# Kernel tuning notes

Hardware: AMD Instinct MI355X
Metric: run time of the kernel (lower is better)

The kernel has to match this reference:

```python
import jax, jax.numpy as jnp
import numpy as np

# Constants from the module source
F_LEN = 1000.0          # focal length (init kwarg f)
C_PP = 512.0            # principal point (init kwarg c)
CAM_SIZE = 1024.0       # camera image_size
H_IMG, W_IMG = 1920 // 8, 1080 // 8   # raster image_size = (240, 135)
SIGMA = 1e-4            # BlendParams.sigma
BLUR = float(np.log(1.0 / 1e-4 - 1.0) * 1e-4)  # blur_radius
V, F = 600, 1000


def setup_inputs() -> dict:
    key = jax.random.key(0)
    k1, k2, k3 = jax.random.split(key, 3)
    # place mesh in front of camera (z ~ 2.5) so it projects on-screen
    verts = jax.random.normal(k1, (V, 3), dtype=jnp.float32) * 0.3 + jnp.array([0.0, 0.0, 2.5], jnp.float32)
    faces = jax.random.randint(k2, (F, 3), 0, V, dtype=jnp.int32)
    gt = (jax.random.uniform(k3, (H_IMG, W_IMG)) > 0.5).astype(jnp.float32)
    return {"verts": verts, "gt": gt, "faces": faces}


def _soft_silhouette(verts, faces):
    # verts: [V,3] camera-space after R flip; faces: [F,3] int
    R = jnp.array([[-1.0, 0.0, 0.0], [0.0, -1.0, 0.0], [0.0, 0.0, 1.0]], verts.dtype)
    v = verts @ R.T                              # == (R @ verts.T).T
    z = jnp.maximum(v[:, 2], 1e-6)
    # pinhole projection to 1024x1024 camera pixels, rescaled to raster grid
    px = (F_LEN * v[:, 0] / z + C_PP) / CAM_SIZE * W_IMG
    py = (F_LEN * v[:, 1] / z + C_PP) / CAM_SIZE * H_IMG
    v2 = jnp.stack([px, py], axis=-1)            # [V,2] raster-pixel coords
    tri = v2[faces]                              # [F,3,2]
    tz = v[:, 2][faces].mean(axis=-1)            # [F] mean depth per face

    ys = jnp.arange(H_IMG, dtype=verts.dtype) + 0.5
    xs = jnp.arange(W_IMG, dtype=verts.dtype) + 0.5
    gy, gx = jnp.meshgrid(ys, xs, indexing="ij")
    p = jnp.stack([gx.ravel(), gy.ravel()], axis=-1)[:, None, :]  # [P,1,2]

    d2min = jnp.full((H_IMG * W_IMG, F), jnp.inf, verts.dtype)
    pos = jnp.ones((H_IMG * W_IMG, F), bool)
    neg = jnp.ones((H_IMG * W_IMG, F), bool)
    for k in range(3):  # fixed loop over 3 triangle edges
        a = tri[None, :, k, :]                   # [1,F,2]
        b = tri[None, :, (k + 1) % 3, :]
        ab = b - a                               # [1,F,2]
        ap = p - a                               # [P,F,2]
        cross = ab[..., 0] * ap[..., 1] - ab[..., 1] * ap[..., 0]
        pos = pos & (cross >= 0)
        neg = neg & (cross <= 0)
        t = jnp.clip((ap * ab).sum(-1) / ((ab * ab).sum(-1) + 1e-12), 0.0, 1.0)
        d2 = ((ap - t[..., None] * ab) ** 2).sum(-1)  # sq dist to edge segment
        d2min = jnp.minimum(d2min, d2)

    inside = pos | neg                           # point-in-triangle test
    signed_d2 = jnp.where(inside, -d2min, d2min) # pytorch3d signed sq distance
    prob = jax.nn.sigmoid(-signed_d2 / SIGMA)    # per-face coverage prob
    valid = (tz > 1e-6)[None, :] & (inside | (d2min <= BLUR))
    prob = jnp.where(valid, prob, 0.0)
    # SoftSilhouetteShader: alpha = 1 - prod_f (1 - prob_f), stable in log space
    alpha = 1.0 - jnp.exp(jnp.sum(jnp.log1p(-prob), axis=1))
    return alpha.reshape(H_IMG, W_IMG)


def reference(verts, gt, faces):
    sil = _soft_silhouette(verts, faces)
    loss = jnp.mean(jnp.abs(sil - gt))
    return loss, sil
```

## Files before the change

### kernel.cpp

```cpp
#include <hip/hip_runtime.h>
#include <math.h>

#define HI 240
#define WI 135
#define NPIX (HI * WI)
#define NF 1000
#define NCHUNK 10
#define FCHUNK (NF / NCHUNK)
#define BLK 256
#define FREC 4
#define TW 8
#define TH 8
#define TX_N 17
#define TY_N 30
#define NTILE (TX_N * TY_N)
#define TPB 4
#define NBX ((NTILE + TPB - 1) / TPB)


__device__ __forceinline__ void project(float x, float y, float z,
                                        float& px, float& py) {
#pragma clang fp contract(off)
    float zc = fmaxf(z, 1e-6f);
    px = ((1000.0f * (-x)) / zc + 512.0f) / 1024.0f * (float)WI;
    py = ((1000.0f * (-y)) / zc + 512.0f) / 1024.0f * (float)HI;
}

__device__ __forceinline__ float eval_face(const float4* sf, int f,
                                           float px, float py)
{
    float4 r0v = sf[FREC * f + 0];
    float4 r1v = sf[FREC * f + 1];
    float4 r2v = sf[FREC * f + 2];
    float4 dv  = sf[FREC * f + 3];

    float a0x = px - r0v.x, a0y = py - r0v.y;
    float a1x = px - r1v.x, a1y = py - r1v.y;
    float a2x = px - r2v.x, a2y = py - r2v.y;

    float c0, c1, c2;
    {
#pragma clang fp contract(off)
        c0 = r0v.z * a0y - r0v.w * a0x;
        c1 = r1v.z * a1y - r1v.w * a1x;
        c2 = r2v.z * a2y - r2v.w * a2x;
    }
    bool pos = (c0 >= 0.0f) & (c1 >= 0.0f) & (c2 >= 0.0f);
    bool neg = (c0 <= 0.0f) & (c1 <= 0.0f) & (c2 <= 0.0f);

    float t0 = fminf(fmaxf((a0x * r0v.z + a0y * r0v.w) * dv.x, 0.0f), 1.0f);
    float t1 = fminf(fmaxf((a1x * r1v.z + a1y * r1v.w) * dv.y, 0.0f), 1.0f);
    float t2 = fminf(fmaxf((a2x * r2v.z + a2y * r2v.w) * dv.z, 0.0f), 1.0f);
    float u0x = a0x - t0 * r0v.z, u0y = a0y - t0 * r0v.w;
    float u1x = a1x - t1 * r1v.z, u1y = a1y - t1 * r1v.w;
    float u2x = a2x - t2 * r2v.z, u2y = a2y - t2 * r2v.w;
    float d20 = u0x * u0x + u0y * u0y;
    float d21 = u1x * u1x + u1y * u1y;
    float d22 = u2x * u2x + u2y * u2y;
    float d2m = fminf(d20, fminf(d21, d22));

    bool inside = pos | neg;
    float uu = (inside ? d2m : -d2m) * 1.0e4f;
    bool valid = (dv.w != 0.0f) & (inside | (d2m <= 9.2102404e-4f));
    float sp;
    if (uu > 16.0f) sp = uu;
    else sp = fmaxf(uu, 0.0f) + __logf(1.0f + __expf(-fabsf(uu)));
    return valid ? sp : 0.0f;
}

__global__ __launch_bounds__(BLK) void sil_kernel(
    const float* __restrict__ verts, const int* __restrict__ faces,
    float* __restrict__ ws, float* __restrict__ out)
{
    __shared__ float4 sf[FCHUNK * FREC];
    __shared__ float sbx0[FCHUNK], sby0[FCHUNK], sbx1[FCHUNK], sby1[FCHUNK];
    __shared__ float sPx[3][FCHUNK], sPy[3][FCHUNK];
    __shared__ float sEx[3][FCHUNK], sEy[3][FCHUNK];
    __shared__ float sRd[3][FCHUNK];
    __shared__ float sFlag[FCHUNK];

    if (blockIdx.x == 0 && blockIdx.y == 0 && threadIdx.x == 0) out[0] = 0.0f;

    {
        int f = threadIdx.x;
        if (f < FCHUNK) {
#pragma clang fp contract(off)
            int g = blockIdx.y * FCHUNK + f;
            int i0 = faces[3 * g + 0], i1 = faces[3 * g + 1], i2 = faces[3 * g + 2];
            float x0 = verts[3 * i0 + 0], y0 = verts[3 * i0 + 1], z0 = verts[3 * i0 + 2];
            float x1 = verts[3 * i1 + 0], y1 = verts[3 * i1 + 1], z1 = verts[3 * i1 + 2];
            float x2 = verts[3 * i2 + 0], y2 = verts[3 * i2 + 1], z2 = verts[3 * i2 + 2];

            float p0x, p0y, p1x, p1y, p2x, p2y;
            project(x0, y0, z0, p0x, p0y);
            project(x1, y1, z1, p1x, p1y);
            project(x2, y2, z2, p2x, p2y);

            float e0x = p1x - p0x, e0y = p1y - p0y;
            float e1x = p2x - p1x, e1y = p2y - p1y;
            float e2x = p0x - p2x, e2y = p0y - p2y;
            float den0 = (e0x * e0x + e0y * e0y) + 1e-12f;
            float den1 = (e1x * e1x + e1y * e1y) + 1e-12f;
            float den2 = (e2x * e2x + e2y * e2y) + 1e-12f;
            float rd0 = 1.0f / den0, rd1 = 1.0f / den1, rd2 = 1.0f / den2;

            float tz = ((z0 + z1) + z2) / 3.0f;
            bool tzok = tz > 1e-6f;

            float orient = e0x * e1y - e0y * e1x;
            float area2 = fabsf(orient);
            float l2max = fmaxf(den0, fmaxf(den1, den2));
            bool dup = (i0 == i1) || (i1 == i2) || (i2 == i0);
            bool patho = dup || (area2 < 4.0e-3f * l2max) || (l2max > 4.0e6f);

            float bx0, by0, bx1, by1, flag;
            if (!tzok) {
                bx0 = 1e30f; by0 = 1e30f; bx1 = -1e30f; by1 = -1e30f; flag = 0.0f;
            } else if (patho) {
                bx0 = -1e30f; by0 = -1e30f; bx1 = 1e30f; by1 = 1e30f; flag = 2.0f;
            } else {
                bx0 = fminf(p0x, fminf(p1x, p2x)) - 0.3f;
                by0 = fminf(p0y, fminf(p1y, p2y)) - 0.3f;
                bx1 = fmaxf(p0x, fmaxf(p1x, p2x)) + 0.3f;
                by1 = fmaxf(p0y, fmaxf(p1y, p2y)) + 0.3f;
                flag = 1.0f;
            }

            sf[FREC * f + 0] = make_float4(p0x, p0y, e0x, e0y);
            sf[FREC * f + 1] = make_float4(p1x, p1y, e1x, e1y);
            sf[FREC * f + 2] = make_float4(p2x, p2y, e2x, e2y);
            sf[FREC * f + 3] = make_float4(rd0, rd1, rd2, tzok ? 1.0f : 0.0f);
            sbx0[f] = bx0; sby0[f] = by0; sbx1[f] = bx1; sby1[f] = by1;
            sFlag[f] = flag;
            float sgn = (orient >= 0.0f) ? 1.0f : -1.0f;
            sPx[0][f] = p0x; sPy[0][f] = p0y; sEx[0][f] = sgn * e0x; sEy[0][f] = sgn * e0y; sRd[0][f] = rd0;
            sPx[1][f] = p1x; sPy[1][f] = p1y; sEx[1][f] = sgn * e1x; sEy[1][f] = sgn * e1y; sRd[1][f] = rd1;
            sPx[2][f] = p2x; sPy[2][f] = p2y; sEx[2][f] = sgn * e2x; sEy[2][f] = sgn * e2y; sRd[2][f] = rd2;
        }
    }
    __syncthreads();

    int wave = threadIdx.x >> 6, lane = threadIdx.x & 63;
    int tile = blockIdx.x * TPB + wave;
    if (tile >= NTILE) return;

    int ty = tile / TX_N, tx = tile - ty * TX_N;
    int col = tx * TW + (lane & 7);
    int row = ty * TH + (lane >> 3);
    bool live = col < WI;
    int q = row * WI + col;
    float px = (float)col + 0.5f;
    float py = (float)row + 0.5f;
    float wx0 = (float)(tx * TW) + 0.5f, wx1 = (float)(tx * TW + TW - 1) + 0.5f;
    float wy0 = (float)(ty * TH) + 0.5f, wy1 = (float)(ty * TH + TH - 1) + 0.5f;

    float sum = live ? 0.0f : -1e30f;
    bool done = false;

    for (int r = 0; r < (FCHUNK + 63) / 64 && !done; ++r) {
        int fl = r * 64 + lane;
        bool ov = false;
        if (fl < FCHUNK) {
            ov = !(sbx0[fl] > wx1 || sbx1[fl] < wx0 ||
                   sby0[fl] > wy1 || sby1[fl] < wy0);
            if (ov && sFlag[fl] == 1.0f) {
                bool cull = false;
#pragma unroll
                for (int k = 0; k < 3; ++k) {
                    float Ex = sEx[k][fl], Ey = sEy[k][fl];
                    float base = Ex * (wy0 - sPy[k][fl]) - Ey * (wx0 - sPx[k][fl]);
                    float mx = base + fmaxf(0.0f, -7.0f * Ey)
                                    + fmaxf(0.0f,  7.0f * Ex);
                    cull |= (mx < 0.0f) & (mx * mx * sRd[k][fl] > 0.09f);
                }
                ov = !cull;
            }
        }
        unsigned long long m = __ballot(ov);

        while (m) {
            int f0 = __ffsll((long long)m) - 1;
            m &= m - 1;
            bool has1 = (m != 0);
            int f1 = has1 ? (__ffsll((long long)m) - 1) : f0;
            if (has1) m &= m - 1;

            float s0 = eval_face(sf, r * 64 + f0, px, py);
            float s1 = eval_face(sf, r * 64 + f1, px, py);
            sum -= s0 + (has1 ? s1 : 0.0f);

            if (__ballot(sum <= -30.0f) == 0xFFFFFFFFFFFFFFFFull) {
                done = true;
                break;
            }
        }
    }
    if (live) ws[(size_t)blockIdx.y * NPIX + q] = sum;
}

__global__ __launch_bounds__(BLK) void fin_kernel(
    const float* __restrict__ ws, const float* __restrict__ gt,
    float* __restrict__ out)
{
    __shared__ float wsum[BLK / 64];
    int q = blockIdx.x * BLK + threadIdx.x;
    float c = 0.0f;
    if (q < NPIX) {
        float s = 0.0f;
        for (int ch = 0; ch < NCHUNK; ++ch) s += ws[(size_t)ch * NPIX + q];
        float alpha = 1.0f - __expf(s);
        out[1 + q] = alpha;
        c = fabsf(alpha - gt[q]);
    }
    for (int off = 32; off > 0; off >>= 1) c += __shfl_down(c, off, 64);
    if ((threadIdx.x & 63) == 0) wsum[threadIdx.x >> 6] = c;
    __syncthreads();
    if (threadIdx.x == 0) {
        float s = 0.0f;
        for (int w = 0; w < BLK / 64; ++w) s += wsum[w];
        atomicAdd(&out[0], s * (1.0f / (float)NPIX));
    }
}

extern "C" void kernel_launch(void* const* d_in, const int* in_sizes, int n_in,
                              void* d_out, int out_size, void* d_ws, size_t ws_size,
                              hipStream_t stream)
{
    const float* verts = (const float*)d_in[0];
    const float* gt    = (const float*)d_in[1];
    const int*   faces = (const int*)d_in[2];
    float* out = (float*)d_out;
    float* ws  = (float*)d_ws;

    dim3 sgrid(NBX, NCHUNK);
    sil_kernel<<<sgrid, BLK, 0, stream>>>(verts, faces, ws, out);

    fin_kernel<<<(NPIX + BLK - 1) / BLK, BLK, 0, stream>>>(ws, gt, out);
}
```

Baseline: 72.41 us.

## Hoist face setup into a prep kernel and double face chunks per pixel tile

Face projection and bounding-box setup move out of every sil_kernel block into a separate prep kernel, which writes per-chunk records to global memory. Each block now just copies its chunk into shared memory. NCHUNK doubles to 20, so each block handles 50 faces in a single 64-lane ballot pass and the grid has twice as many blocks. This removes redundant per-block setup work and adds parallelism, at the cost of one extra kernel launch and twice the workspace traffic in fin_kernel.

New measurement: 77.96 us. 7.7% more time.

```diff
diff --git a/kernel.cpp b/kernel.cpp
--- a/kernel.cpp
+++ b/kernel.cpp
@@ -5,7 +5,7 @@
 #define WI 135
 #define NPIX (HI * WI)
 #define NF 1000
-#define NCHUNK 10
+#define NCHUNK 20
 #define FCHUNK (NF / NCHUNK)
 #define BLK 256
 #define FREC 4
@@ -17,6 +17,11 @@
 #define TPB 4
 #define NBX ((NTILE + TPB - 1) / TPB)
 
+#define CH_EVAL (FCHUNK * FREC)
+#define NSCAN 20
+#define CH_SCAN_F (NSCAN * FCHUNK)
+#define CH_SCAN_V (CH_SCAN_F / 4)
+
 
 __device__ __forceinline__ void project(float x, float y, float z,
                                         float& px, float& py) {
@@ -24,6 +29,74 @@
     float zc = fmaxf(z, 1e-6f);
     px = ((1000.0f * (-x)) / zc + 512.0f) / 1024.0f * (float)WI;
     py = ((1000.0f * (-y)) / zc + 512.0f) / 1024.0f * (float)HI;
+}
+
+__global__ __launch_bounds__(BLK) void prep_kernel(
+    const float* __restrict__ verts, const int* __restrict__ faces,
+    float* __restrict__ out, float4* __restrict__ gA, float* __restrict__ gS)
+{
+#pragma clang fp contract(off)
+    int g = blockIdx.x * BLK + threadIdx.x;
+    if (g == 0) out[0] = 0.0f;
+    if (g >= NF) return;
+
+    int i0 = faces[3 * g + 0], i1 = faces[3 * g + 1], i2 = faces[3 * g + 2];
+    float x0 = verts[3 * i0 + 0], y0 = verts[3 * i0 + 1], z0 = verts[3 * i0 + 2];
+    float x1 = verts[3 * i1 + 0], y1 = verts[3 * i1 + 1], z1 = verts[3 * i1 + 2];
+    float x2 = verts[3 * i2 + 0], y2 = verts[3 * i2 + 1], z2 = verts[3 * i2 + 2];
+
+    float p0x, p0y, p1x, p1y, p2x, p2y;
+    project(x0, y0, z0, p0x, p0y);
+    project(x1, y1, z1, p1x, p1y);
+    project(x2, y2, z2, p2x, p2y);
+
+    float e0x = p1x - p0x, e0y = p1y - p0y;
+    float e1x = p2x - p1x, e1y = p2y - p1y;
+    float e2x = p0x - p2x, e2y = p0y - p2y;
+    float den0 = (e0x * e0x + e0y * e0y) + 1e-12f;
+    float den1 = (e1x * e1x + e1y * e1y) + 1e-12f;
+    float den2 = (e2x * e2x + e2y * e2y) + 1e-12f;
+    float rd0 = 1.0f / den0, rd1 = 1.0f / den1, rd2 = 1.0f / den2;
+
+    float tz = ((z0 + z1) + z2) / 3.0f;
+    bool tzok = tz > 1e-6f;
+
+    float orient = e0x * e1y - e0y * e1x;
+    float area2 = fabsf(orient);
+    float l2max = fmaxf(den0, fmaxf(den1, den2));
+    bool dup = (i0 == i1) || (i1 == i2) || (i2 == i0);
+    bool patho = dup || (area2 < 4.0e-3f * l2max) || (l2max > 4.0e6f);
+
+    float bx0, by0, bx1, by1, flag;
+    if (!tzok) {
+        bx0 = 1e30f; by0 = 1e30f; bx1 = -1e30f; by1 = -1e30f; flag = 0.0f;
+    } else if (patho) {
+        bx0 = -1e30f; by0 = -1e30f; bx1 = 1e30f; by1 = 1e30f; flag = 2.0f;
+    } else {
+        bx0 = fminf(p0x, fminf(p1x, p2x)) - 0.3f;
+        by0 = fminf(p0y, fminf(p1y, p2y)) - 0.3f;
+        bx1 = fmaxf(p0x, fmaxf(p1x, p2x)) + 0.3f;
+        by1 = fmaxf(p0y, fmaxf(p1y, p2y)) + 0.3f;
+        flag = 1.0f;
+    }
+
+    int c = g / FCHUNK, f = g - c * FCHUNK;
+    float4* ga = gA + (size_t)c * CH_EVAL;
+    ga[4 * f + 0] = make_float4(p0x, p0y, e0x, e0y);
+    ga[4 * f + 1] = make_float4(p1x, p1y, e1x, e1y);
+    ga[4 * f + 2] = make_float4(p2x, p2y, e2x, e2y);
+    ga[4 * f + 3] = make_float4(rd0, rd1, rd2, tzok ? 1.0f : 0.0f);
+
+    float* gs = gS + (size_t)c * CH_SCAN_F;
+    float sgn = (orient >= 0.0f) ? 1.0f : -1.0f;
+    gs[0 * FCHUNK + f] = bx0;  gs[1 * FCHUNK + f] = by0;
+    gs[2 * FCHUNK + f] = bx1;  gs[3 * FCHUNK + f] = by1;
+    gs[4 * FCHUNK + f] = flag;
+    gs[5 * FCHUNK + f] = p0x;  gs[6 * FCHUNK + f] = p1x;  gs[7 * FCHUNK + f] = p2x;
+    gs[8 * FCHUNK + f] = p0y;  gs[9 * FCHUNK + f] = p1y;  gs[10 * FCHUNK + f] = p2y;
+    gs[11 * FCHUNK + f] = sgn * e0x; gs[12 * FCHUNK + f] = sgn * e1x; gs[13 * FCHUNK + f] = sgn * e2x;
+    gs[14 * FCHUNK + f] = sgn * e0y; gs[15 * FCHUNK + f] = sgn * e1y; gs[16 * FCHUNK + f] = sgn * e2y;
+    gs[17 * FCHUNK + f] = rd0; gs[18 * FCHUNK + f] = rd1; gs[19 * FCHUNK + f] = rd2;
 }
 
 __device__ __forceinline__ float eval_face(const float4* sf, int f,
@@ -69,73 +142,19 @@
 }
 
 __global__ __launch_bounds__(BLK) void sil_kernel(
-    const float* __restrict__ verts, const int* __restrict__ faces,
-    float* __restrict__ ws, float* __restrict__ out)
-{
-    __shared__ float4 sf[FCHUNK * FREC];
-    __shared__ float sbx0[FCHUNK], sby0[FCHUNK], sbx1[FCHUNK], sby1[FCHUNK];
-    __shared__ float sPx[3][FCHUNK], sPy[3][FCHUNK];
-    __shared__ float sEx[3][FCHUNK], sEy[3][FCHUNK];
-    __shared__ float sRd[3][FCHUNK];
-    __shared__ float sFlag[FCHUNK];
-
-    if (blockIdx.x == 0 && blockIdx.y == 0 && threadIdx.x == 0) out[0] = 0.0f;
+    const float4* __restrict__ gA, const float* __restrict__ gS,
+    float* __restrict__ ws)
+{
+    __shared__ float4 sf[CH_EVAL];
+    __shared__ float4 sscan4[CH_SCAN_V];
+    const float* ss = (const float*)sscan4;
 
     {
-        int f = threadIdx.x;
-        if (f < FCHUNK) {
-#pragma clang fp contract(off)
-            int g = blockIdx.y * FCHUNK + f;
-            int i0 = faces[3 * g + 0], i1 = faces[3 * g + 1], i2 = faces[3 * g + 2];
-            float x0 = verts[3 * i0 + 0], y0 = verts[3 * i0 + 1], z0 = verts[3 * i0 + 2];
-            float x1 = verts[3 * i1 + 0], y1 = verts[3 * i1 + 1], z1 = verts[3 * i1 + 2];
-            float x2 = verts[3 * i2 + 0], y2 = verts[3 * i2 + 1], z2 = verts[3 * i2 + 2];
-
-            float p0x, p0y, p1x, p1y, p2x, p2y;
-            project(x0, y0, z0, p0x, p0y);
-            project(x1, y1, z1, p1x, p1y);
-            project(x2, y2, z2, p2x, p2y);
-
-            float e0x = p1x - p0x, e0y = p1y - p0y;
-            float e1x = p2x - p1x, e1y = p2y - p1y;
-            float e2x = p0x - p2x, e2y = p0y - p2y;
-            float den0 = (e0x * e0x + e0y * e0y) + 1e-12f;
-            float den1 = (e1x * e1x + e1y * e1y) + 1e-12f;
-            float den2 = (e2x * e2x + e2y * e2y) + 1e-12f;
-            float rd0 = 1.0f / den0, rd1 = 1.0f / den1, rd2 = 1.0f / den2;
-
-            float tz = ((z0 + z1) + z2) / 3.0f;
-            bool tzok = tz > 1e-6f;
-
-            float orient = e0x * e1y - e0y * e1x;
-            float area2 = fabsf(orient);
-            float l2max = fmaxf(den0, fmaxf(den1, den2));
-            bool dup = (i0 == i1) || (i1 == i2) || (i2 == i0);
-            bool patho = dup || (area2 < 4.0e-3f * l2max) || (l2max > 4.0e6f);
-
-            float bx0, by0, bx1, by1, flag;
-            if (!tzok) {
-                bx0 = 1e30f; by0 = 1e30f; bx1 = -1e30f; by1 = -1e30f; flag = 0.0f;
-            } else if (patho) {
-                bx0 = -1e30f; by0 = -1e30f; bx1 = 1e30f; by1 = 1e30f; flag = 2.0f;
-            } else {
-                bx0 = fminf(p0x, fminf(p1x, p2x)) - 0.3f;
-                by0 = fminf(p0y, fminf(p1y, p2y)) - 0.3f;
-                bx1 = fmaxf(p0x, fmaxf(p1x, p2x)) + 0.3f;
-                by1 = fmaxf(p0y, fmaxf(p1y, p2y)) + 0.3f;
-                flag = 1.0f;
-            }
-
-            sf[FREC * f + 0] = make_float4(p0x, p0y, e0x, e0y);
-            sf[FREC * f + 1] = make_float4(p1x, p1y, e1x, e1y);
-            sf[FREC * f + 2] = make_float4(p2x, p2y, e2x, e2y);
-            sf[FREC * f + 3] = make_float4(rd0, rd1, rd2, tzok ? 1.0f : 0.0f);
-            sbx0[f] = bx0; sby0[f] = by0; sbx1[f] = bx1; sby1[f] = by1;
-            sFlag[f] = flag;
-            float sgn = (orient >= 0.0f) ? 1.0f : -1.0f;
-            sPx[0][f] = p0x; sPy[0][f] = p0y; sEx[0][f] = sgn * e0x; sEy[0][f] = sgn * e0y; sRd[0][f] = rd0;
-            sPx[1][f] = p1x; sPy[1][f] = p1y; sEx[1][f] = sgn * e1x; sEy[1][f] = sgn * e1y; sRd[1][f] = rd1;
-            sPx[2][f] = p2x; sPy[2][f] = p2y; sEx[2][f] = sgn * e2x; sEy[2][f] = sgn * e2y; sRd[2][f] = rd2;
+        const float4* ga = gA + (size_t)blockIdx.y * CH_EVAL;
+        const float4* gs4 = (const float4*)gS + (size_t)blockIdx.y * CH_SCAN_V;
+        for (int i = threadIdx.x; i < CH_EVAL + CH_SCAN_V; i += BLK) {
+            if (i < CH_EVAL) sf[i] = ga[i];
+            else             sscan4[i - CH_EVAL] = gs4[i - CH_EVAL];
         }
     }
     __syncthreads();
@@ -155,45 +174,41 @@
     float wy0 = (float)(ty * TH) + 0.5f, wy1 = (float)(ty * TH + TH - 1) + 0.5f;
 
     float sum = live ? 0.0f : -1e30f;
-    bool done = false;
-
-    for (int r = 0; r < (FCHUNK + 63) / 64 && !done; ++r) {
-        int fl = r * 64 + lane;
-        bool ov = false;
-        if (fl < FCHUNK) {
-            ov = !(sbx0[fl] > wx1 || sbx1[fl] < wx0 ||
-                   sby0[fl] > wy1 || sby1[fl] < wy0);
-            if (ov && sFlag[fl] == 1.0f) {
-                bool cull = false;
+
+    bool ov = false;
+    if (lane < FCHUNK) {
+        int fl = lane;
+        ov = !(ss[0 * FCHUNK + fl] > wx1 || ss[2 * FCHUNK + fl] < wx0 ||
+               ss[1 * FCHUNK + fl] > wy1 || ss[3 * FCHUNK + fl] < wy0);
+        if (ov && ss[4 * FCHUNK + fl] == 1.0f) {
+            bool cull = false;
 #pragma unroll
-                for (int k = 0; k < 3; ++k) {
-                    float Ex = sEx[k][fl], Ey = sEy[k][fl];
-                    float base = Ex * (wy0 - sPy[k][fl]) - Ey * (wx0 - sPx[k][fl]);
-                    float mx = base + fmaxf(0.0f, -7.0f * Ey)
-                                    + fmaxf(0.0f,  7.0f * Ex);
-                    cull |= (mx < 0.0f) & (mx * mx * sRd[k][fl] > 0.09f);
-                }
-                ov = !cull;
+            for (int k = 0; k < 3; ++k) {
+                float Ex = ss[(11 + k) * FCHUNK + fl];
+                float Ey = ss[(14 + k) * FCHUNK + fl];
+                float base = Ex * (wy0 - ss[(8 + k) * FCHUNK + fl])
+                           - Ey * (wx0 - ss[(5 + k) * FCHUNK + fl]);
+                float mx = base + fmaxf(0.0f, -7.0f * Ey)
+                                + fmaxf(0.0f,  7.0f * Ex);
+                cull |= (mx < 0.0f) & (mx * mx * ss[(17 + k) * FCHUNK + fl] > 0.09f);
             }
+            ov = !cull;
         }
-        unsigned long long m = __ballot(ov);
-
-        while (m) {
-            int f0 = __ffsll((long long)m) - 1;
-            m &= m - 1;
-            bool has1 = (m != 0);
-            int f1 = has1 ? (__ffsll((long long)m) - 1) : f0;
-            if (has1) m &= m - 1;
-
-            float s0 = eval_face(sf, r * 64 + f0, px, py);
-            float s1 = eval_face(sf, r * 64 + f1, px, py);
-            sum -= s0 + (has1 ? s1 : 0.0f);
-
-            if (__ballot(sum <= -30.0f) == 0xFFFFFFFFFFFFFFFFull) {
-                done = true;
-                break;
-            }
-        }
+    }
+    unsigned long long m = __ballot(ov);
+
+    while (m) {
+        int f0 = __ffsll((long long)m) - 1;
+        m &= m - 1;
+        bool has1 = (m != 0);
+        int f1 = has1 ? (__ffsll((long long)m) - 1) : f0;
+        if (has1) m &= m - 1;
+
+        float s0 = eval_face(sf, f0, px, py);
+        float s1 = eval_face(sf, f1, px, py);
+        sum -= s0 + (has1 ? s1 : 0.0f);
+
+        if (__ballot(sum <= -30.0f) == 0xFFFFFFFFFFFFFFFFull) break;
     }
     if (live) ws[(size_t)blockIdx.y * NPIX + q] = sum;
 }
@@ -230,10 +245,16 @@
     const float* gt    = (const float*)d_in[1];
     const int*   faces = (const int*)d_in[2];
     float* out = (float*)d_out;
-    float* ws  = (float*)d_ws;
+
+    char* w = (char*)d_ws;
+    float* ws = (float*)w;
+    float4* gA = (float4*)(w + (size_t)NCHUNK * NPIX * 4);
+    float* gS  = (float*)((char*)gA + (size_t)NF * FREC * 16);
+
+    prep_kernel<<<(NF + BLK - 1) / BLK, BLK, 0, stream>>>(verts, faces, out, gA, gS);
 
     dim3 sgrid(NBX, NCHUNK);
-    sil_kernel<<<sgrid, BLK, 0, stream>>>(verts, faces, ws, out);
+    sil_kernel<<<sgrid, BLK, 0, stream>>>(gA, gS, ws);
 
     fin_kernel<<<(NPIX + BLK - 1) / BLK, BLK, 0, stream>>>(ws, gt, out);
 }
```

## Process all faces per block and fuse alpha/loss into silhouette kernel

Applied to the files above, without the earlier changes.

Drops the split of faces into 10 chunks across grid y. Each block now projects and bins all 1000 faces into a 14-row SoA shared array and runs the whole face loop per tile. It then computes alpha and the per-pixel abs error directly, writes per-block partial sums, and a one-block kernel does a deterministic final reduction without atomics. Edges are recomputed from vertices in eval_face to save shared memory. This removes the workspace round-trip and gives early termination across all faces, but cuts grid parallelism tenfold (128 blocks instead of 1280) and makes every block redo projection for all faces.

Measured after the change: 86.83 us. 19.9% more time.

```diff
diff --git a/kernel.cpp b/kernel.cpp
--- a/kernel.cpp
+++ b/kernel.cpp
@@ -5,10 +5,7 @@
 #define WI 135
 #define NPIX (HI * WI)
 #define NF 1000
-#define NCHUNK 10
-#define FCHUNK (NF / NCHUNK)
 #define BLK 256
-#define FREC 4
 #define TW 8
 #define TH 8
 #define TX_N 17
@@ -26,34 +23,38 @@
     py = ((1000.0f * (-y)) / zc + 512.0f) / 1024.0f * (float)HI;
 }
 
-__device__ __forceinline__ float eval_face(const float4* sf, int f,
+__device__ __forceinline__ float eval_face(const float S[14][NF], int f,
                                            float px, float py)
 {
-    float4 r0v = sf[FREC * f + 0];
-    float4 r1v = sf[FREC * f + 1];
-    float4 r2v = sf[FREC * f + 2];
-    float4 dv  = sf[FREC * f + 3];
-
-    float a0x = px - r0v.x, a0y = py - r0v.y;
-    float a1x = px - r1v.x, a1y = py - r1v.y;
-    float a2x = px - r2v.x, a2y = py - r2v.y;
+    float p0x = S[5][f], p0y = S[6][f];
+    float p1x = S[7][f], p1y = S[8][f];
+    float p2x = S[9][f], p2y = S[10][f];
+    float rd0 = S[11][f], rd1 = S[12][f], rd2 = S[13][f];
+
+    float e0x = p1x - p0x, e0y = p1y - p0y;
+    float e1x = p2x - p1x, e1y = p2y - p1y;
+    float e2x = p0x - p2x, e2y = p0y - p2y;
+
+    float a0x = px - p0x, a0y = py - p0y;
+    float a1x = px - p1x, a1y = py - p1y;
+    float a2x = px - p2x, a2y = py - p2y;
 
     float c0, c1, c2;
     {
 #pragma clang fp contract(off)
-        c0 = r0v.z * a0y - r0v.w * a0x;
-        c1 = r1v.z * a1y - r1v.w * a1x;
-        c2 = r2v.z * a2y - r2v.w * a2x;
+        c0 = e0x * a0y - e0y * a0x;
+        c1 = e1x * a1y - e1y * a1x;
+        c2 = e2x * a2y - e2y * a2x;
     }
     bool pos = (c0 >= 0.0f) & (c1 >= 0.0f) & (c2 >= 0.0f);
     bool neg = (c0 <= 0.0f) & (c1 <= 0.0f) & (c2 <= 0.0f);
 
-    float t0 = fminf(fmaxf((a0x * r0v.z + a0y * r0v.w) * dv.x, 0.0f), 1.0f);
-    float t1 = fminf(fmaxf((a1x * r1v.z + a1y * r1v.w) * dv.y, 0.0f), 1.0f);
-    float t2 = fminf(fmaxf((a2x * r2v.z + a2y * r2v.w) * dv.z, 0.0f), 1.0f);
-    float u0x = a0x - t0 * r0v.z, u0y = a0y - t0 * r0v.w;
-    float u1x = a1x - t1 * r1v.z, u1y = a1y - t1 * r1v.w;
-    float u2x = a2x - t2 * r2v.z, u2y = a2y - t2 * r2v.w;
+    float t0 = fminf(fmaxf((a0x * e0x + a0y * e0y) * rd0, 0.0f), 1.0f);
+    float t1 = fminf(fmaxf((a1x * e1x + a1y * e1y) * rd1, 0.0f), 1.0f);
+    float t2 = fminf(fmaxf((a2x * e2x + a2y * e2y) * rd2, 0.0f), 1.0f);
+    float u0x = a0x - t0 * e0x, u0y = a0y - t0 * e0y;
+    float u1x = a1x - t1 * e1x, u1y = a1y - t1 * e1y;
+    float u2x = a2x - t2 * e2x, u2y = a2y - t2 * e2y;
     float d20 = u0x * u0x + u0y * u0y;
     float d21 = u1x * u1x + u1y * u1y;
     float d22 = u2x * u2x + u2y * u2y;
@@ -61,7 +62,7 @@
 
     bool inside = pos | neg;
     float uu = (inside ? d2m : -d2m) * 1.0e4f;
-    bool valid = (dv.w != 0.0f) & (inside | (d2m <= 9.2102404e-4f));
+    bool valid = inside | (d2m <= 9.2102404e-4f);
     float sp;
     if (uu > 16.0f) sp = uu;
     else sp = fmaxf(uu, 0.0f) + __logf(1.0f + __expf(-fabsf(uu)));
@@ -70,155 +71,156 @@
 
 __global__ __launch_bounds__(BLK) void sil_kernel(
     const float* __restrict__ verts, const int* __restrict__ faces,
-    float* __restrict__ ws, float* __restrict__ out)
-{
-    __shared__ float4 sf[FCHUNK * FREC];
-    __shared__ float sbx0[FCHUNK], sby0[FCHUNK], sbx1[FCHUNK], sby1[FCHUNK];
-    __shared__ float sPx[3][FCHUNK], sPy[3][FCHUNK];
-    __shared__ float sEx[3][FCHUNK], sEy[3][FCHUNK];
-    __shared__ float sRd[3][FCHUNK];
-    __shared__ float sFlag[FCHUNK];
-
-    if (blockIdx.x == 0 && blockIdx.y == 0 && threadIdx.x == 0) out[0] = 0.0f;
-
-    {
-        int f = threadIdx.x;
-        if (f < FCHUNK) {
+    const float* __restrict__ gt, float* __restrict__ out,
+    float* __restrict__ ws)
+{
+    __shared__ float S[14][NF];
+    __shared__ float wsum[TPB];
+
+    for (int f = threadIdx.x; f < NF; f += BLK) {
 #pragma clang fp contract(off)
-            int g = blockIdx.y * FCHUNK + f;
-            int i0 = faces[3 * g + 0], i1 = faces[3 * g + 1], i2 = faces[3 * g + 2];
-            float x0 = verts[3 * i0 + 0], y0 = verts[3 * i0 + 1], z0 = verts[3 * i0 + 2];
-            float x1 = verts[3 * i1 + 0], y1 = verts[3 * i1 + 1], z1 = verts[3 * i1 + 2];
-            float x2 = verts[3 * i2 + 0], y2 = verts[3 * i2 + 1], z2 = verts[3 * i2 + 2];
-
-            float p0x, p0y, p1x, p1y, p2x, p2y;
-            project(x0, y0, z0, p0x, p0y);
-            project(x1, y1, z1, p1x, p1y);
-            project(x2, y2, z2, p2x, p2y);
-
-            float e0x = p1x - p0x, e0y = p1y - p0y;
-            float e1x = p2x - p1x, e1y = p2y - p1y;
-            float e2x = p0x - p2x, e2y = p0y - p2y;
-            float den0 = (e0x * e0x + e0y * e0y) + 1e-12f;
-            float den1 = (e1x * e1x + e1y * e1y) + 1e-12f;
-            float den2 = (e2x * e2x + e2y * e2y) + 1e-12f;
-            float rd0 = 1.0f / den0, rd1 = 1.0f / den1, rd2 = 1.0f / den2;
-
-            float tz = ((z0 + z1) + z2) / 3.0f;
-            bool tzok = tz > 1e-6f;
-
-            float orient = e0x * e1y - e0y * e1x;
-            float area2 = fabsf(orient);
-            float l2max = fmaxf(den0, fmaxf(den1, den2));
-            bool dup = (i0 == i1) || (i1 == i2) || (i2 == i0);
-            bool patho = dup || (area2 < 4.0e-3f * l2max) || (l2max > 4.0e6f);
-
-            float bx0, by0, bx1, by1, flag;
-            if (!tzok) {
-                bx0 = 1e30f; by0 = 1e30f; bx1 = -1e30f; by1 = -1e30f; flag = 0.0f;
-            } else if (patho) {
-                bx0 = -1e30f; by0 = -1e30f; bx1 = 1e30f; by1 = 1e30f; flag = 2.0f;
-            } else {
-                bx0 = fminf(p0x, fminf(p1x, p2x)) - 0.3f;
-                by0 = fminf(p0y, fminf(p1y, p2y)) - 0.3f;
-                bx1 = fmaxf(p0x, fmaxf(p1x, p2x)) + 0.3f;
-                by1 = fmaxf(p0y, fmaxf(p1y, p2y)) + 0.3f;
-                flag = 1.0f;
-            }
-
-            sf[FREC * f + 0] = make_float4(p0x, p0y, e0x, e0y);
-            sf[FREC * f + 1] = make_float4(p1x, p1y, e1x, e1y);
-            sf[FREC * f + 2] = make_float4(p2x, p2y, e2x, e2y);
-            sf[FREC * f + 3] = make_float4(rd0, rd1, rd2, tzok ? 1.0f : 0.0f);
-            sbx0[f] = bx0; sby0[f] = by0; sbx1[f] = bx1; sby1[f] = by1;
-            sFlag[f] = flag;
-            float sgn = (orient >= 0.0f) ? 1.0f : -1.0f;
-            sPx[0][f] = p0x; sPy[0][f] = p0y; sEx[0][f] = sgn * e0x; sEy[0][f] = sgn * e0y; sRd[0][f] = rd0;
-            sPx[1][f] = p1x; sPy[1][f] = p1y; sEx[1][f] = sgn * e1x; sEy[1][f] = sgn * e1y; sRd[1][f] = rd1;
-            sPx[2][f] = p2x; sPy[2][f] = p2y; sEx[2][f] = sgn * e2x; sEy[2][f] = sgn * e2y; sRd[2][f] = rd2;
+        int i0 = faces[3 * f + 0], i1 = faces[3 * f + 1], i2 = faces[3 * f + 2];
+        float x0 = verts[3 * i0 + 0], y0 = verts[3 * i0 + 1], z0 = verts[3 * i0 + 2];
+        float x1 = verts[3 * i1 + 0], y1 = verts[3 * i1 + 1], z1 = verts[3 * i1 + 2];
+        float x2 = verts[3 * i2 + 0], y2 = verts[3 * i2 + 1], z2 = verts[3 * i2 + 2];
+
+        float p0x, p0y, p1x, p1y, p2x, p2y;
+        project(x0, y0, z0, p0x, p0y);
+        project(x1, y1, z1, p1x, p1y);
+        project(x2, y2, z2, p2x, p2y);
+
+        float e0x = p1x - p0x, e0y = p1y - p0y;
+        float e1x = p2x - p1x, e1y = p2y - p1y;
+        float e2x = p0x - p2x, e2y = p0y - p2y;
+        float den0 = (e0x * e0x + e0y * e0y) + 1e-12f;
+        float den1 = (e1x * e1x + e1y * e1y) + 1e-12f;
+        float den2 = (e2x * e2x + e2y * e2y) + 1e-12f;
+
+        float tz = ((z0 + z1) + z2) / 3.0f;
+        bool tzok = tz > 1e-6f;
+
+        float orient = e0x * e1y - e0y * e1x;
+        float area2 = fabsf(orient);
+        float l2max = fmaxf(den0, fmaxf(den1, den2));
+        bool dup = (i0 == i1) || (i1 == i2) || (i2 == i0);
+        bool patho = dup || (area2 < 4.0e-3f * l2max) || (l2max > 4.0e6f);
+
+        float bx0, by0, bx1, by1, flag;
+        if (!tzok) {
+            bx0 = 1e30f; by0 = 1e30f; bx1 = -1e30f; by1 = -1e30f; flag = 0.0f;
+        } else if (patho) {
+            bx0 = -1e30f; by0 = -1e30f; bx1 = 1e30f; by1 = 1e30f; flag = 2.0f;
+        } else {
+            bx0 = fminf(p0x, fminf(p1x, p2x)) - 0.3f;
+            by0 = fminf(p0y, fminf(p1y, p2y)) - 0.3f;
+            bx1 = fmaxf(p0x, fmaxf(p1x, p2x)) + 0.3f;
+            by1 = fmaxf(p0y, fmaxf(p1y, p2y)) + 0.3f;
+            flag = (orient >= 0.0f) ? 1.0f : -1.0f;
         }
+
+        S[0][f] = bx0;  S[1][f] = by0;  S[2][f] = bx1;  S[3][f] = by1;
+        S[4][f] = flag;
+        S[5][f] = p0x;  S[6][f] = p0y;
+        S[7][f] = p1x;  S[8][f] = p1y;
+        S[9][f] = p2x;  S[10][f] = p2y;
+        S[11][f] = 1.0f / den0;  S[12][f] = 1.0f / den1;  S[13][f] = 1.0f / den2;
     }
     __syncthreads();
 
     int wave = threadIdx.x >> 6, lane = threadIdx.x & 63;
     int tile = blockIdx.x * TPB + wave;
-    if (tile >= NTILE) return;
-
-    int ty = tile / TX_N, tx = tile - ty * TX_N;
-    int col = tx * TW + (lane & 7);
-    int row = ty * TH + (lane >> 3);
-    bool live = col < WI;
-    int q = row * WI + col;
-    float px = (float)col + 0.5f;
-    float py = (float)row + 0.5f;
-    float wx0 = (float)(tx * TW) + 0.5f, wx1 = (float)(tx * TW + TW - 1) + 0.5f;
-    float wy0 = (float)(ty * TH) + 0.5f, wy1 = (float)(ty * TH + TH - 1) + 0.5f;
-
-    float sum = live ? 0.0f : -1e30f;
-    bool done = false;
-
-    for (int r = 0; r < (FCHUNK + 63) / 64 && !done; ++r) {
-        int fl = r * 64 + lane;
-        bool ov = false;
-        if (fl < FCHUNK) {
-            ov = !(sbx0[fl] > wx1 || sbx1[fl] < wx0 ||
-                   sby0[fl] > wy1 || sby1[fl] < wy0);
-            if (ov && sFlag[fl] == 1.0f) {
-                bool cull = false;
+    bool wave_active = tile < NTILE;
+
+    float c = 0.0f;
+    if (wave_active) {
+        int ty = tile / TX_N, tx = tile - ty * TX_N;
+        int col = tx * TW + (lane & 7);
+        int row = ty * TH + (lane >> 3);
+        bool live = col < WI;
+        int q = row * WI + col;
+        float px = (float)col + 0.5f;
+        float py = (float)row + 0.5f;
+        float wx0 = (float)(tx * TW) + 0.5f, wx1 = (float)(tx * TW + TW - 1) + 0.5f;
+        float wy0 = (float)(ty * TH) + 0.5f, wy1 = (float)(ty * TH + TH - 1) + 0.5f;
+
+        float sum = live ? 0.0f : -1e30f;
+        bool done = false;
+
+        for (int r = 0; r < (NF + 63) / 64 && !done; ++r) {
+            int fl = r * 64 + lane;
+            bool ov = false;
+            if (fl < NF) {
+                ov = !(S[0][fl] > wx1 || S[2][fl] < wx0 ||
+                       S[1][fl] > wy1 || S[3][fl] < wy0);
+                float flg = S[4][fl];
+                if (ov && flg != 2.0f) {
+                    float sgn = flg;
+                    bool cull = false;
 #pragma unroll
-                for (int k = 0; k < 3; ++k) {
-                    float Ex = sEx[k][fl], Ey = sEy[k][fl];
-                    float base = Ex * (wy0 - sPy[k][fl]) - Ey * (wx0 - sPx[k][fl]);
-                    float mx = base + fmaxf(0.0f, -7.0f * Ey)
-                                    + fmaxf(0.0f,  7.0f * Ex);
-                    cull |= (mx < 0.0f) & (mx * mx * sRd[k][fl] > 0.09f);
+                    for (int k = 0; k < 3; ++k) {
+                        int kn = (k == 2) ? 0 : (k + 1);
+                        float Px = S[5 + 2 * k][fl], Py = S[6 + 2 * k][fl];
+                        float Ex = S[5 + 2 * kn][fl] - Px;
+                        float Ey = S[6 + 2 * kn][fl] - Py;
+                        float sEx = sgn * Ex, sEy = sgn * Ey;
+                        float base = sEx * (wy0 - Py) - sEy * (wx0 - Px);
+                        float mx = base + fmaxf(0.0f, -7.0f * sEy)
+                                        + fmaxf(0.0f,  7.0f * sEx);
+                        cull |= (mx < 0.0f) & (mx * mx * S[11 + k][fl] > 0.09f);
+                    }
+                    ov = !cull;
                 }
-                ov = !cull;
+            }
+            unsigned long long m = __ballot(ov);
+
+            while (m) {
+                int f0 = r * 64 + (__ffsll((long long)m) - 1);
+                m &= m - 1;
+                bool has1 = (m != 0);
+                int f1 = has1 ? (r * 64 + __ffsll((long long)m) - 1) : f0;
+                if (has1) m &= m - 1;
+
+                float s0 = eval_face(S, f0, px, py);
+                float s1 = eval_face(S, f1, px, py);
+                sum -= s0 + (has1 ? s1 : 0.0f);
+
+                if (__ballot(sum <= -30.0f) == 0xFFFFFFFFFFFFFFFFull) {
+                    done = true;
+                    break;
+                }
             }
         }
-        unsigned long long m = __ballot(ov);
-
-        while (m) {
-            int f0 = __ffsll((long long)m) - 1;
-            m &= m - 1;
-            bool has1 = (m != 0);
-            int f1 = has1 ? (__ffsll((long long)m) - 1) : f0;
-            if (has1) m &= m - 1;
-
-            float s0 = eval_face(sf, r * 64 + f0, px, py);
-            float s1 = eval_face(sf, r * 64 + f1, px, py);
-            sum -= s0 + (has1 ? s1 : 0.0f);
-
-            if (__ballot(sum <= -30.0f) == 0xFFFFFFFFFFFFFFFFull) {
-                done = true;
-                break;
-            }
+
+        if (live) {
+            float alpha = 1.0f - __expf(sum);
+            out[1 + q] = alpha;
+            c = fabsf(alpha - gt[q]);
         }
     }
-    if (live) ws[(size_t)blockIdx.y * NPIX + q] = sum;
-}
-
-__global__ __launch_bounds__(BLK) void fin_kernel(
-    const float* __restrict__ ws, const float* __restrict__ gt,
-    float* __restrict__ out)
-{
-    __shared__ float wsum[BLK / 64];
-    int q = blockIdx.x * BLK + threadIdx.x;
-    float c = 0.0f;
-    if (q < NPIX) {
-        float s = 0.0f;
-        for (int ch = 0; ch < NCHUNK; ++ch) s += ws[(size_t)ch * NPIX + q];
-        float alpha = 1.0f - __expf(s);
-        out[1 + q] = alpha;
-        c = fabsf(alpha - gt[q]);
-    }
+
     for (int off = 32; off > 0; off >>= 1) c += __shfl_down(c, off, 64);
-    if ((threadIdx.x & 63) == 0) wsum[threadIdx.x >> 6] = c;
+    if (lane == 0) wsum[wave] = c;
     __syncthreads();
     if (threadIdx.x == 0) {
         float s = 0.0f;
+        for (int w = 0; w < TPB; ++w) s += wsum[w];
+        ws[blockIdx.x] = s;
+    }
+}
+
+__global__ __launch_bounds__(BLK) void fin2_kernel(
+    const float* __restrict__ ws, float* __restrict__ out)
+{
+    __shared__ float wsum[BLK / 64];
+    int t = threadIdx.x;
+    float c = (t < NBX) ? ws[t] : 0.0f;
+    for (int off = 32; off > 0; off >>= 1) c += __shfl_down(c, off, 64);
+    if ((t & 63) == 0) wsum[t >> 6] = c;
+    __syncthreads();
+    if (t == 0) {
+        float s = 0.0f;
         for (int w = 0; w < BLK / 64; ++w) s += wsum[w];
-        atomicAdd(&out[0], s * (1.0f / (float)NPIX));
+        out[0] = s * (1.0f / (float)NPIX);
     }
 }
 
@@ -232,8 +234,6 @@
     float* out = (float*)d_out;
     float* ws  = (float*)d_ws;
 
-    dim3 sgrid(NBX, NCHUNK);
-    sil_kernel<<<sgrid, BLK, 0, stream>>>(verts, faces, ws, out);
-
-    fin_kernel<<<(NPIX + BLK - 1) / BLK, BLK, 0, stream>>>(ws, gt, out);
-}
+    sil_kernel<<<NBX, BLK, 0, stream>>>(verts, faces, gt, out, ws);
+    fin2_kernel<<<1, BLK, 0, stream>>>(ws, out);
+}
```
